# Kernel tuning notes

Hardware: AMD Instinct MI355X
Metric: run time of the kernel (lower is better)

Reference implementation:

```python
import jax, jax.numpy as jnp
import numpy as np
from jax import lax

# Static module config (matches init_kwargs)
KH, KW = 3, 3
SH, SW = 1, 1
PH, PW = 1, 1
DH, DW = 1, 1
DG = 1           # deformable groups
GROUPS = 1


def setup_inputs() -> dict:
    key = jax.random.key(0)
    k1, k2, k3 = jax.random.split(key, 3)
    B, C, H, W = 8, 256, 64, 64
    Co = 256
    K = KH * KW
    x = jax.random.normal(k1, (B, C, H, W), dtype=jnp.float32)
    # offset/mask conv weight: (2+1)*DG*K = 27 output channels; small so offsets are a few pixels
    w_offset = jax.random.normal(k2, (3 * DG * K, C, KH, KW), dtype=jnp.float32) * 0.05
    # main conv weight, uniform(-stdv, stdv) per reset_parameters
    stdv = 1.0 / np.sqrt(C * KH * KW)
    w_conv = jax.random.uniform(k3, (Co, C, KH, KW), dtype=jnp.float32, minval=-stdv, maxval=stdv)
    return {"input_feat": x, "w_offset": w_offset, "w_conv": w_conv}


def _bilinear_gather(x, py, px):
    """x: (B, DG, Cg, H, W); py/px: (B, DG, K, Ho, Wo) float sample coords.
    Returns sampled values (B, DG, Cg, K, Ho, Wo) with zero padding outside."""
    B, dg, Cg, H, W = x.shape
    _, _, K, Ho, Wo = py.shape
    xf = x.reshape(B, dg, Cg, H * W)

    y0 = jnp.floor(py)
    x0 = jnp.floor(px)
    ly = py - y0
    lx = px - x0
    y0i = y0.astype(jnp.int32)
    x0i = x0.astype(jnp.int32)
    y1i = y0i + 1
    x1i = x0i + 1

    def gather(yi, xi):
        valid = (yi >= 0) & (yi < H) & (xi >= 0) & (xi < W)
        idx = jnp.clip(yi, 0, H - 1) * W + jnp.clip(xi, 0, W - 1)  # (B,dg,K,Ho,Wo)
        idx_f = idx.reshape(B, dg, K * Ho * Wo)
        g = jax.vmap(jax.vmap(lambda f, i: jnp.take(f, i, axis=1)))(xf, idx_f)
        return g.reshape(B, dg, Cg, K, Ho, Wo), valid

    g00, v00 = gather(y0i, x0i)
    g01, v01 = gather(y0i, x1i)
    g10, v10 = gather(y1i, x0i)
    g11, v11 = gather(y1i, x1i)

    w00 = ((1 - ly) * (1 - lx) * v00)[:, :, None]
    w01 = ((1 - ly) * lx * v01)[:, :, None]
    w10 = (ly * (1 - lx) * v10)[:, :, None]
    w11 = (ly * lx * v11)[:, :, None]
    return g00 * w00 + g01 * w01 + g10 * w10 + g11 * w11


def _deform_conv(x, w_offset, w_conv):
    B, C, H, W = x.shape
    Co = w_conv.shape[0]
    K = KH * KW
    dn = ("NCHW", "OIHW", "NCHW")

    # offset/mask branch (regular conv)
    om = lax.conv_general_dilated(x, w_offset, (SH, SW), ((PH, PH), (PW, PW)),
                                  rhs_dilation=(DH, DW), dimension_numbers=dn)
    Ho, Wo = om.shape[2], om.shape[3]
    off_y = om[:, : DG * K].reshape(B, DG, K, Ho, Wo)
    off_x = om[:, DG * K: 2 * DG * K].reshape(B, DG, K, Ho, Wo)
    mask = jax.nn.sigmoid(om[:, 2 * DG * K:]).reshape(B, DG, 1, K, Ho, Wo)

    # base sampling grid
    oy = jnp.arange(Ho) * SH - PH                 # (Ho,)
    ox = jnp.arange(Wo) * SW - PW                 # (Wo,)
    ky = (jnp.arange(KH) * DH)[:, None].repeat(KW, 1).reshape(K)  # (K,)
    kx = (jnp.arange(KW) * DW)[None, :].repeat(KH, 0).reshape(K)  # (K,)
    py = ky[None, None, :, None, None] + oy[None, None, None, :, None] + off_y
    px = kx[None, None, :, None, None] + ox[None, None, None, None, :] + off_x

    xg = x.reshape(B, DG, C // DG, H, W)
    sampled = _bilinear_gather(xg, py, px) * mask  # (B,DG,Cg,K,Ho,Wo)

    cols = sampled.reshape(B, C, K, Ho * Wo)
    wk = w_conv.reshape(Co, C, K)
    out = jnp.einsum("bckn,ock->bon", cols, wk)
    return out.reshape(B, Co, Ho, Wo)


def reference(input_feat, w_offset, w_conv):
    return _deform_conv(input_feat, w_offset, w_conv)
```

## Files before the change

kernel.cpp:

```cpp
#include <hip/hip_runtime.h>
#include <hip/hip_bf16.h>

typedef float f32x4 __attribute__((ext_vector_type(4)));
typedef unsigned int u32x4 __attribute__((ext_vector_type(4)));
typedef __bf16 bf16x8 __attribute__((ext_vector_type(8)));

#define NSP 4096
#define KTOT 2304

static __device__ __forceinline__ float bflo(unsigned u) {
  return __builtin_bit_cast(float, u << 16);
}
static __device__ __forceinline__ float bfhi(unsigned u) {
  return __builtin_bit_cast(float, u & 0xffff0000u);
}
static __device__ __forceinline__ unsigned short bfbits(float f) {
  return __builtin_bit_cast(unsigned short, (__bf16)f);
}
static __device__ __forceinline__ unsigned packbf2(float f0, float f1) {
  return (unsigned)bfbits(f0) | ((unsigned)bfbits(f1) << 16);
}
static __device__ __forceinline__ float bf16f(unsigned short h) {
  return __builtin_bit_cast(float, (unsigned)h << 16);
}

__global__ __launch_bounds__(256) void k_nhwc(const float* __restrict__ x,
                                              unsigned short* __restrict__ XH) {
  const int by = blockIdx.x;
  const int t = threadIdx.x;
  const int xw = t & 63;
  const int cq = t >> 6;
  const float* xp = x + (((by >> 6) * 256 * 64 + (by & 63)) * 64 + xw);
  unsigned short* oh = XH + (by * 64 + xw) * 256;
#pragma unroll
  for (int j8 = 0; j8 < 8; ++j8) {
    const int c0 = cq * 64 + j8 * 8;
    u32x4 vh;
#pragma unroll
    for (int d = 0; d < 4; ++d) {
      float f0 = xp[(c0 + 2 * d) * 4096];
      float f1 = xp[(c0 + 2 * d + 1) * 4096];
      vh[d] = packbf2(f0, f1);
    }
    *(u32x4*)(oh + c0) = vh;
  }
}

__global__ void k_wprep_all(const float* __restrict__ wc, const float* __restrict__ wof,
                            unsigned short* __restrict__ AW2,
                            unsigned short* __restrict__ AF) {
  int idx = blockIdx.x * 256 + threadIdx.x;
  if (idx < 589824) {
    int ks = idx / 16384;
    int r = idx - ks * 16384;
    int chunk = r >> 5;
    int e = r & 31;
    int ah = chunk >> 8, am = chunk & 255;
    int col = (ks >> 2) * 256 + (ks & 3) * 64 + ah * 32 + e;
    int c = col & 255, tap = col >> 8;
    AW2[idx] = bfbits(wc[(am * 256 + c) * 9 + tap]);
  } else {
    int j = idx - 589824;
    if (j < 147456) {
      int skc = j >> 11;
      int r = j & 2047;
      int fi = r >> 9;
      int lane = (r >> 3) & 63;
      int e = r & 7;
      int ks = skc >> 1, kc = skc & 1;
      int tap = ks >> 2, q = ks & 3;
      int mr = lane & 15, ko = (lane >> 4) * 8;
      int m = (fi & 1) * 16 + mr;
      int gcol = tap * 256 + q * 64 + ko + kc * 32 + e;
      int c = gcol & 255;
      int t = gcol >> 8;
      float v = (m < 27) ? wof[(m * 256 + c) * 9 + t] : 0.f;
      unsigned short h = bfbits(v);
      AF[j] = (fi >> 1) ? bfbits(v - bf16f(h)) : h;
    }
  }
}

__global__ __launch_bounds__(256) void k_offc2(const unsigned short* __restrict__ AF,
                                               const unsigned short* __restrict__ XH,
                                               f32x4* __restrict__ W4,
                                               unsigned* __restrict__ C4) {
  __shared__ u32x4 ldsq[1024];
  unsigned char* ldsbase = (unsigned char*)ldsq;
  float* lds32 = (float*)ldsq;

  const int tid = threadIdx.x;
  const int bid = blockIdx.x;
  const int b = bid & 7;
  const int y = bid >> 3;
  const int l = tid & 63;
  const int w = tid >> 6;

  const unsigned short* xb = XH + b * (64 * 64 * 256);
  const int sp = tid >> 2;
  const int qtr = tid & 3;
  const unsigned swb = (unsigned)(sp & 7) << 4;
  const int col = w * 16 + (l & 15);
  const unsigned swc = (unsigned)(col & 7) << 4;

  f32x4 acc0 = (f32x4){0.f, 0.f, 0.f, 0.f};
  f32x4 acc1 = (f32x4){0.f, 0.f, 0.f, 0.f};
  u32x4 v0, v1;

  {
    const int yy = y - 1;
    const int xx = sp - 1;
    const bool valid = ((unsigned)yy < 64u) & ((unsigned)xx < 64u);
    const int yyc = min(max(yy, 0), 63), xxc = min(max(xx, 0), 63);
    const unsigned short* src = xb + ((yyc * 64 + xxc) * 256 + qtr * 16);
    u32x4 z = (u32x4){0u, 0u, 0u, 0u};
    v0 = valid ? *(const u32x4*)src : z;
    v1 = valid ? *(const u32x4*)(src + 8) : z;
    *(u32x4*)(ldsbase + (unsigned)sp * 128u + (((unsigned)(qtr * 32)) ^ swb)) = v0;
    *(u32x4*)(ldsbase + (unsigned)sp * 128u + (((unsigned)(qtr * 32 + 16)) ^ swb)) = v1;
  }

  for (int ks = 0; ks < 36; ++ks) {
    unsigned char* ldsB = ldsbase + (ks & 1) * 8192;
    unsigned char* ldsBn = ldsbase + ((ks & 1) ^ 1) * 8192;
    const bool pf = (ks + 1 < 36);

    if (pf) {
      int tap = (ks + 1) >> 2, q = (ks + 1) & 3;
      int yy = y + tap / 3 - 1, xx = sp + tap % 3 - 1;
      bool valid = ((unsigned)yy < 64u) & ((unsigned)xx < 64u);
      int yyc = min(max(yy, 0), 63), xxc = min(max(xx, 0), 63);
      const unsigned short* src = xb + ((yyc * 64 + xxc) * 256 + q * 64 + qtr * 16);
      u32x4 z = (u32x4){0u, 0u, 0u, 0u};
      v0 = valid ? *(const u32x4*)src : z;
      v1 = valid ? *(const u32x4*)(src + 8) : z;
    }

    asm volatile("s_waitcnt lgkmcnt(0)" ::: "memory");
    __builtin_amdgcn_s_barrier();

    const unsigned short* af = AF + ks * 4096;
#pragma unroll
    for (int kc = 0; kc < 2; ++kc) {
      bf16x8 ah0 = *(const bf16x8*)(af + kc * 2048 + l * 8);
      bf16x8 ah1 = *(const bf16x8*)(af + kc * 2048 + 512 + l * 8);
      bf16x8 al0 = *(const bf16x8*)(af + kc * 2048 + 1024 + l * 8);
      bf16x8 al1 = *(const bf16x8*)(af + kc * 2048 + 1536 + l * 8);
      bf16x8 bh = *(const bf16x8*)(ldsB + (unsigned)col * 128u +
                                   (((unsigned)(kc * 64 + (l >> 4) * 16)) ^ swc));
      acc0 = __builtin_amdgcn_mfma_f32_16x16x32_bf16(ah0, bh, acc0, 0, 0, 0);
      acc1 = __builtin_amdgcn_mfma_f32_16x16x32_bf16(ah1, bh, acc1, 0, 0, 0);
      acc0 = __builtin_amdgcn_mfma_f32_16x16x32_bf16(al0, bh, acc0, 0, 0, 0);
      acc1 = __builtin_amdgcn_mfma_f32_16x16x32_bf16(al1, bh, acc1, 0, 0, 0);
    }

    if (pf) {
      *(u32x4*)(ldsBn + (unsigned)sp * 128u + (((unsigned)(qtr * 32)) ^ swb)) = v0;
      *(u32x4*)(ldsBn + (unsigned)sp * 128u + (((unsigned)(qtr * 32 + 16)) ^ swb)) = v1;
    }
  }

  __syncthreads();
#pragma unroll
  for (int mf = 0; mf < 2; ++mf) {
    f32x4 a = mf ? acc1 : acc0;
#pragma unroll
    for (int r = 0; r < 4; ++r) {
      int m = mf * 16 + (l >> 4) * 4 + r;
      int px = w * 16 + (l & 15);
      lds32[m * 64 + px] = a[r];
    }
  }
  __syncthreads();

#pragma unroll
  for (int it = 0; it < 3; ++it) {
    int idx = tid + it * 256;
    if (idx < 9 * 64) {
      int k = idx >> 6, px = idx & 63;
      float oy = lds32[k * 64 + px];
      float ox = lds32[(9 + k) * 64 + px];
      float lg = lds32[(18 + k) * 64 + px];
      int s = y * 64 + px;
      float py = oy + (float)y - 1.f + (float)(k / 3);
      float pxf = ox + (float)px - 1.f + (float)(k % 3);
      float mk = 1.f / (1.f + __expf(-lg));

      float y0f = floorf(py), x0f = floorf(pxf);
      float ly = py - y0f, lx = pxf - x0f;
      int y0 = (int)y0f, x0 = (int)x0f;
      int y1 = y0 + 1, x1 = x0 + 1;
      float omy = 1.f - ly, omx = 1.f - lx;
      bool y0v = (unsigned)y0 < 64u, y1v = (unsigned)y1 < 64u;
      bool x0v = (unsigned)x0 < 64u, x1v = (unsigned)x1 < 64u;
      f32x4 wv;
      wv[0] = (y0v && x0v) ? omy * omx * mk : 0.f;
      wv[1] = (y0v && x1v) ? omy * lx * mk : 0.f;
      wv[2] = (y1v && x0v) ? ly * omx * mk : 0.f;
      wv[3] = (y1v && x1v) ? ly * lx * mk : 0.f;
      int y0c = min(max(y0, 0), 63), y1c = min(max(y1, 0), 63);
      int x0c = min(max(x0, 0), 63), x1c = min(max(x1, 0), 63);
      unsigned p00 = (unsigned)(y0c * 64 + x0c);
      unsigned p11 = (unsigned)(y1c * 64 + x1c);
      int ci = (b * 9 + k) * NSP + s;
      W4[ci] = wv;
      C4[ci] = p00 | (p11 << 16);
    }
  }
}

struct Bld16 {
  u32x4 g00a, g00b, g01a, g01b, g10a, g10b, g11a, g11b;
  f32x4 wv;
};

static __device__ __forceinline__ void loadB16(const unsigned short* __restrict__ xb,
                                               const f32x4* __restrict__ W4,
                                               const unsigned* __restrict__ C4,
                                               int b, int k, int c0, int bc, int s,
                                               Bld16& r) {
  int ci = (b * 9 + k) * NSP + s;
  r.wv = W4[ci];
  unsigned c4 = C4[ci];
  unsigned p00 = c4 & 0xffffu, p11 = c4 >> 16;
  unsigned p01 = (p00 & ~63u) | (p11 & 63u);
  unsigned p10 = (p11 & ~63u) | (p00 & 63u);
  const unsigned short* base = xb + (c0 + bc);
  const unsigned short* q00 = base + (p00 << 8);
  const unsigned short* q01 = base + (p01 << 8);
  const unsigned short* q10 = base + (p10 << 8);
  const unsigned short* q11 = base + (p11 << 8);
  r.g00a = *(const u32x4*)q00;
  r.g00b = *(const u32x4*)(q00 + 8);
  r.g01a = *(const u32x4*)q01;
  r.g01b = *(const u32x4*)(q01 + 8);
  r.g10a = *(const u32x4*)q10;
  r.g10b = *(const u32x4*)(q10 + 8);
  r.g11a = *(const u32x4*)q11;
  r.g11b = *(const u32x4*)(q11 + 8);
}

static __device__ __forceinline__ void blendB16(const Bld16& r, u32x4& o0, u32x4& o1) {
#pragma unroll
  for (int d = 0; d < 4; ++d) {
    float a0 = r.wv[0] * bflo(r.g00a[d]) + r.wv[1] * bflo(r.g01a[d]) +
               r.wv[2] * bflo(r.g10a[d]) + r.wv[3] * bflo(r.g11a[d]);
    float a1 = r.wv[0] * bfhi(r.g00a[d]) + r.wv[1] * bfhi(r.g01a[d]) +
               r.wv[2] * bfhi(r.g10a[d]) + r.wv[3] * bfhi(r.g11a[d]);
    o0[d] = packbf2(a0, a1);
    float b0 = r.wv[0] * bflo(r.g00b[d]) + r.wv[1] * bflo(r.g01b[d]) +
               r.wv[2] * bflo(r.g10b[d]) + r.wv[3] * bflo(r.g11b[d]);
    float b1 = r.wv[0] * bfhi(r.g00b[d]) + r.wv[1] * bfhi(r.g01b[d]) +
               r.wv[2] * bfhi(r.g10b[d]) + r.wv[3] * bfhi(r.g11b[d]);
    o1[d] = packbf2(b0, b1);
  }
}

__global__ __launch_bounds__(512) void k_gemm(const unsigned short* __restrict__ AW2,
                                              const unsigned short* __restrict__ XH,
                                              const f32x4* __restrict__ W4,
                                              const unsigned* __restrict__ C4,
                                              float* __restrict__ out) {
  __shared__ u32x4 lds2[2][3072];
  unsigned char* ldsbase = (unsigned char*)lds2;

  const int tid = threadIdx.x;
  const int bid = blockIdx.x;
  const int b = bid & 7;
  const int s0 = (bid >> 3) * 128;

  const int l = tid & 63;
  const int w = tid >> 6;
  const int wm = (w >> 1) * 64;
  const int wn = (w & 1) * 64;

  const int am = tid & 255;
  const int ah = tid >> 8;
  const unsigned swa = (unsigned)(am & 7) << 4;

  const int bn = tid >> 2;
  const int bc = (tid & 3) * 16;
  const int s = s0 + bn;
  const unsigned swb = (unsigned)(bn & 7) << 4;
  const unsigned short* xb = XH + b * (64 * 64 * 256);

  f32x4 acc[4][4];
#pragma unroll
  for (int i = 0; i < 4; ++i)
#pragma unroll
    for (int j = 0; j < 4; ++j) acc[i][j] = (f32x4){0.f, 0.f, 0.f, 0.f};

  u32x4 ar[4];
  u32x4 o0, o1;
  Bld16 bld;

#pragma unroll
  for (int j = 0; j < 4; ++j)
    ar[j] = *(const u32x4*)(AW2 + tid * 32 + j * 8);
  loadB16(xb, W4, C4, b, 0, 0, bc, s, bld);
  blendB16(bld, o0, o1);
  {
    unsigned char* ldsA = ldsbase;
    unsigned char* ldsB = ldsbase + 32768;
    const unsigned abase = (unsigned)am * 128u;
#pragma unroll
    for (int j = 0; j < 4; ++j)
      *(u32x4*)(ldsA + abase + (((unsigned)(ah * 64 + j * 16)) ^ swa)) = ar[j];
    const unsigned bbase = (unsigned)bn * 128u;
    *(u32x4*)(ldsB + bbase + (((unsigned)(bc * 2)) ^ swb)) = o0;
    *(u32x4*)(ldsB + bbase + (((unsigned)(bc * 2 + 16)) ^ swb)) = o1;
  }

  for (int ks = 0; ks < 36; ++ks) {
    const int cur = ks & 1;
    unsigned char* ldsA = ldsbase + cur * 49152;
    unsigned char* ldsB = ldsA + 32768;
    unsigned char* ldsAn = ldsbase + (cur ^ 1) * 49152;
    unsigned char* ldsBn = ldsAn + 32768;

    asm volatile("s_waitcnt lgkmcnt(0)" ::: "memory");
    __builtin_amdgcn_s_barrier();

    const int kn = (ks + 1) >> 2, cn = ((ks + 1) & 3) << 6;

    if (ks + 1 < 36) {
#pragma unroll
      for (int j = 0; j < 4; ++j)
        ar[j] = *(const u32x4*)(AW2 + (ks + 1) * 16384 + tid * 32 + j * 8);
    }

    __builtin_amdgcn_s_setprio(1);
    {
      bf16x8 af[4], bfr[4];
      const unsigned co = (unsigned)((l >> 4) * 16);
#pragma unroll
      for (int i = 0; i < 4; ++i) {
        int row = wm + i * 16 + (l & 15);
        af[i] = *(const bf16x8*)(ldsA + (unsigned)row * 128u +
                                 (co ^ ((unsigned)(row & 7) << 4)));
      }
#pragma unroll
      for (int j = 0; j < 4; ++j) {
        int col = wn + j * 16 + (l & 15);
        bfr[j] = *(const bf16x8*)(ldsB + (unsigned)col * 128u +
                                  (co ^ ((unsigned)(col & 7) << 4)));
      }
#pragma unroll
      for (int i = 0; i < 4; ++i)
#pragma unroll
        for (int j = 0; j < 4; ++j)
          acc[i][j] = __builtin_amdgcn_mfma_f32_16x16x32_bf16(af[i], bfr[j],
                                                              acc[i][j], 0, 0, 0);
    }
    __builtin_amdgcn_s_setprio(0);

    if (ks + 1 < 36) loadB16(xb, W4, C4, b, kn, cn, bc, s, bld);

    __builtin_amdgcn_s_setprio(1);
    {
      bf16x8 af[4], bfr[4];
      const unsigned co = (unsigned)(64 + (l >> 4) * 16);
#pragma unroll
      for (int i = 0; i < 4; ++i) {
        int row = wm + i * 16 + (l & 15);
        af[i] = *(const bf16x8*)(ldsA + (unsigned)row * 128u +
                                 (co ^ ((unsigned)(row & 7) << 4)));
      }
#pragma unroll
      for (int j = 0; j < 4; ++j) {
        int col = wn + j * 16 + (l & 15);
        bfr[j] = *(const bf16x8*)(ldsB + (unsigned)col * 128u +
                                  (co ^ ((unsigned)(col & 7) << 4)));
      }
#pragma unroll
      for (int i = 0; i < 4; ++i)
#pragma unroll
        for (int j = 0; j < 4; ++j)
          acc[i][j] = __builtin_amdgcn_mfma_f32_16x16x32_bf16(af[i], bfr[j],
                                                              acc[i][j], 0, 0, 0);
    }
    __builtin_amdgcn_s_setprio(0);

    if (ks + 1 < 36) {
      blendB16(bld, o0, o1);
      const unsigned abase = (unsigned)am * 128u;
#pragma unroll
      for (int j = 0; j < 4; ++j)
        *(u32x4*)(ldsAn + abase + (((unsigned)(ah * 64 + j * 16)) ^ swa)) = ar[j];
      const unsigned bbase = (unsigned)bn * 128u;
      *(u32x4*)(ldsBn + bbase + (((unsigned)(bc * 2)) ^ swb)) = o0;
      *(u32x4*)(ldsBn + bbase + (((unsigned)(bc * 2 + 16)) ^ swb)) = o1;
    }
  }

  const int cn2 = l & 15;
  const int r0 = (l >> 4) * 4;
#pragma unroll
  for (int i = 0; i < 4; ++i) {
#pragma unroll
    for (int j = 0; j < 4; ++j) {
      int sc = s0 + wn + j * 16 + cn2;
#pragma unroll
      for (int r = 0; r < 4; ++r) {
        int o = wm + i * 16 + r0 + r;
        out[((b * 256 + o) << 12) + sc] = acc[i][j][r];
      }
    }
  }
}

extern "C" void kernel_launch(void* const* d_in, const int* in_sizes, int n_in,
                              void* d_out, int out_size, void* d_ws, size_t ws_size,
                              hipStream_t stream) {
  const float* x = (const float*)d_in[0];
  const float* wof = (const float*)d_in[1];
  const float* wc = (const float*)d_in[2];
  float* out = (float*)d_out;
  char* ws = (char*)d_ws;

  unsigned short* XH = (unsigned short*)(ws);
  unsigned short* AW2 = (unsigned short*)(ws + 16777216);
  unsigned short* AF = (unsigned short*)(ws + 17956864);
  f32x4* W4 = (f32x4*)(ws + 18251776);
  unsigned* C4 = (unsigned*)(ws + 22970368);

  k_nhwc<<<512, 256, 0, stream>>>(x, XH);
  k_wprep_all<<<2880, 256, 0, stream>>>(wc, wof, AW2, AF);
  k_offc2<<<512, 256, 0, stream>>>(AF, XH, W4, C4);
  k_gemm<<<256, 512, 0, stream>>>(AW2, XH, W4, C4, out);
}
```

Baseline: 126.5 us.

## Deepen global prefetch pipeline to two stages with decoupled metadata loads

Splits the B-operand load into a metadata load (weights and corner indices) and a corner gather. The main loop is unrolled by two with ping-pong register sets so that the gather for step ks+2 and the metadata for ks+3 are issued while step ks computes. This is meant to hide the dependent latency chain from metadata load to corner gather, and the global load latency in general, behind the MFMA work. The cost is roughly double the register state for prefetch buffers, which may raise VGPR pressure or cause spills at 512 threads per block.

```diff
diff --git a/kernel.cpp b/kernel.cpp
--- a/kernel.cpp
+++ b/kernel.cpp
@@ -214,14 +214,19 @@
   f32x4 wv;
 };
 
-static __device__ __forceinline__ void loadB16(const unsigned short* __restrict__ xb,
-                                               const f32x4* __restrict__ W4,
-                                               const unsigned* __restrict__ C4,
-                                               int b, int k, int c0, int bc, int s,
-                                               Bld16& r) {
+static __device__ __forceinline__ void loadMeta(const f32x4* __restrict__ W4,
+                                                const unsigned* __restrict__ C4,
+                                                int b, int k, int s,
+                                                f32x4& wv, unsigned& c4) {
   int ci = (b * 9 + k) * NSP + s;
-  r.wv = W4[ci];
-  unsigned c4 = C4[ci];
+  wv = W4[ci];
+  c4 = C4[ci];
+}
+
+static __device__ __forceinline__ void loadCorners(const unsigned short* __restrict__ xb,
+                                                   f32x4 wv, unsigned c4, int c0, int bc,
+                                                   Bld16& r) {
+  r.wv = wv;
   unsigned p00 = c4 & 0xffffu, p11 = c4 >> 16;
   unsigned p01 = (p00 & ~63u) | (p11 & 63u);
   unsigned p10 = (p11 & ~63u) | (p00 & 63u);
@@ -259,7 +264,7 @@
 __global__ __launch_bounds__(512) void k_gemm(const unsigned short* __restrict__ AW2,
                                               const unsigned short* __restrict__ XH,
                                               const f32x4* __restrict__ W4,
-                                              const unsigned* __restrict__ C4,
+                                              const unsigned* __restrict__ C4v,
                                               float* __restrict__ out) {
   __shared__ u32x4 lds2[2][3072];
   unsigned char* ldsbase = (unsigned char*)lds2;
@@ -290,107 +295,104 @@
 #pragma unroll
     for (int j = 0; j < 4; ++j) acc[i][j] = (f32x4){0.f, 0.f, 0.f, 0.f};
 
-  u32x4 ar[4];
-  u32x4 o0, o1;
-  Bld16 bld;
-
-#pragma unroll
-  for (int j = 0; j < 4; ++j)
-    ar[j] = *(const u32x4*)(AW2 + tid * 32 + j * 8);
-  loadB16(xb, W4, C4, b, 0, 0, bc, s, bld);
-  blendB16(bld, o0, o1);
+  f32x4 mwvA, mwvB;
+  unsigned mc4A, mc4B;
+  Bld16 bldA, bldB;
+  u32x4 arA[4], arB[4];
+
+  loadMeta(W4, C4v, b, 0, s, mwvA, mc4A);
+  loadMeta(W4, C4v, b, 0, s, mwvB, mc4B);
+#pragma unroll
+  for (int j = 0; j < 4; ++j) arA[j] = *(const u32x4*)(AW2 + tid * 32 + j * 8);
+  loadCorners(xb, mwvA, mc4A, 0, bc, bldA);
+  loadMeta(W4, C4v, b, 0, s, mwvA, mc4A);
   {
+    u32x4 o0, o1;
+    blendB16(bldA, o0, o1);
     unsigned char* ldsA = ldsbase;
     unsigned char* ldsB = ldsbase + 32768;
     const unsigned abase = (unsigned)am * 128u;
 #pragma unroll
     for (int j = 0; j < 4; ++j)
-      *(u32x4*)(ldsA + abase + (((unsigned)(ah * 64 + j * 16)) ^ swa)) = ar[j];
+      *(u32x4*)(ldsA + abase + (((unsigned)(ah * 64 + j * 16)) ^ swa)) = arA[j];
     const unsigned bbase = (unsigned)bn * 128u;
     *(u32x4*)(ldsB + bbase + (((unsigned)(bc * 2)) ^ swb)) = o0;
     *(u32x4*)(ldsB + bbase + (((unsigned)(bc * 2 + 16)) ^ swb)) = o1;
   }
-
-  for (int ks = 0; ks < 36; ++ks) {
-    const int cur = ks & 1;
+#pragma unroll
+  for (int j = 0; j < 4; ++j)
+    arB[j] = *(const u32x4*)(AW2 + 16384 + tid * 32 + j * 8);
+  loadCorners(xb, mwvB, mc4B, 64, bc, bldB);
+
+  auto mfma_half = [&](unsigned char* ldsA, unsigned char* ldsB, int H) {
+    bf16x8 af[4], bfr[4];
+    const unsigned co = (unsigned)(H * 64 + ((l >> 4) * 16));
+#pragma unroll
+    for (int i = 0; i < 4; ++i) {
+      int row = wm + i * 16 + (l & 15);
+      af[i] = *(const bf16x8*)(ldsA + (unsigned)row * 128u +
+                               (co ^ ((unsigned)(row & 7) << 4)));
+    }
+#pragma unroll
+    for (int j = 0; j < 4; ++j) {
+      int col = wn + j * 16 + (l & 15);
+      bfr[j] = *(const bf16x8*)(ldsB + (unsigned)col * 128u +
+                                (co ^ ((unsigned)(col & 7) << 4)));
+    }
+#pragma unroll
+    for (int i = 0; i < 4; ++i)
+#pragma unroll
+      for (int j = 0; j < 4; ++j)
+        acc[i][j] = __builtin_amdgcn_mfma_f32_16x16x32_bf16(af[i], bfr[j],
+                                                            acc[i][j], 0, 0, 0);
+  };
+
+  auto gstep = [&](int KS, u32x4 (&arI)[4], Bld16& bldI, f32x4& mwvI, unsigned& mc4I,
+                   f32x4& mwvO, unsigned& mc4O, u32x4 (&arU)[4], Bld16& bldU) {
+    const int cur = KS & 1;
     unsigned char* ldsA = ldsbase + cur * 49152;
     unsigned char* ldsB = ldsA + 32768;
     unsigned char* ldsAn = ldsbase + (cur ^ 1) * 49152;
     unsigned char* ldsBn = ldsAn + 32768;
 
+    if (KS + 2 < 36) {
+#pragma unroll
+      for (int j = 0; j < 4; ++j)
+        arI[j] = *(const u32x4*)(AW2 + (KS + 2) * 16384 + tid * 32 + j * 8);
+    }
+
     asm volatile("s_waitcnt lgkmcnt(0)" ::: "memory");
     __builtin_amdgcn_s_barrier();
 
-    const int kn = (ks + 1) >> 2, cn = ((ks + 1) & 3) << 6;
-
-    if (ks + 1 < 36) {
+    __builtin_amdgcn_s_setprio(1);
+    mfma_half(ldsA, ldsB, 0);
+    __builtin_amdgcn_s_setprio(0);
+
+    if (KS + 2 < 36)
+      loadCorners(xb, mwvI, mc4I, ((KS + 2) & 3) << 6, bc, bldI);
+    if (KS + 3 < 36)
+      loadMeta(W4, C4v, b, (KS + 3) >> 2, s, mwvO, mc4O);
+
+    __builtin_amdgcn_s_setprio(1);
+    mfma_half(ldsA, ldsB, 1);
+    __builtin_amdgcn_s_setprio(0);
+
+    if (KS + 1 < 36) {
+      u32x4 o0, o1;
+      blendB16(bldU, o0, o1);
+      const unsigned abase = (unsigned)am * 128u;
 #pragma unroll
       for (int j = 0; j < 4; ++j)
-        ar[j] = *(const u32x4*)(AW2 + (ks + 1) * 16384 + tid * 32 + j * 8);
-    }
-
-    __builtin_amdgcn_s_setprio(1);
-    {
-      bf16x8 af[4], bfr[4];
-      const unsigned co = (unsigned)((l >> 4) * 16);
-#pragma unroll
-      for (int i = 0; i < 4; ++i) {
-        int row = wm + i * 16 + (l & 15);
-        af[i] = *(const bf16x8*)(ldsA + (unsigned)row * 128u +
-                                 (co ^ ((unsigned)(row & 7) << 4)));
-      }
-#pragma unroll
-      for (int j = 0; j < 4; ++j) {
-        int col = wn + j * 16 + (l & 15);
-        bfr[j] = *(const bf16x8*)(ldsB + (unsigned)col * 128u +
-                                  (co ^ ((unsigned)(col & 7) << 4)));
-      }
-#pragma unroll
-      for (int i = 0; i < 4; ++i)
-#pragma unroll
-        for (int j = 0; j < 4; ++j)
-          acc[i][j] = __builtin_amdgcn_mfma_f32_16x16x32_bf16(af[i], bfr[j],
-                                                              acc[i][j], 0, 0, 0);
-    }
-    __builtin_amdgcn_s_setprio(0);
-
-    if (ks + 1 < 36) loadB16(xb, W4, C4, b, kn, cn, bc, s, bld);
-
-    __builtin_amdgcn_s_setprio(1);
-    {
-      bf16x8 af[4], bfr[4];
-      const unsigned co = (unsigned)(64 + (l >> 4) * 16);
-#pragma unroll
-      for (int i = 0; i < 4; ++i) {
-        int row = wm + i * 16 + (l & 15);
-        af[i] = *(const bf16x8*)(ldsA + (unsigned)row * 128u +
-                                 (co ^ ((unsigned)(row & 7) << 4)));
-      }
-#pragma unroll
-      for (int j = 0; j < 4; ++j) {
-        int col = wn + j * 16 + (l & 15);
-        bfr[j] = *(const bf16x8*)(ldsB + (unsigned)col * 128u +
-                                  (co ^ ((unsigned)(col & 7) << 4)));
-      }
-#pragma unroll
-      for (int i = 0; i < 4; ++i)
-#pragma unroll
-        for (int j = 0; j < 4; ++j)
-          acc[i][j] = __builtin_amdgcn_mfma_f32_16x16x32_bf16(af[i], bfr[j],
-                                                              acc[i][j], 0, 0, 0);
-    }
-    __builtin_amdgcn_s_setprio(0);
-
-    if (ks + 1 < 36) {
-      blendB16(bld, o0, o1);
-      const unsigned abase = (unsigned)am * 128u;
-#pragma unroll
-      for (int j = 0; j < 4; ++j)
-        *(u32x4*)(ldsAn + abase + (((unsigned)(ah * 64 + j * 16)) ^ swa)) = ar[j];
+        *(u32x4*)(ldsAn + abase + (((unsigned)(ah * 64 + j * 16)) ^ swa)) = arU[j];
       const unsigned bbase = (unsigned)bn * 128u;
       *(u32x4*)(ldsBn + bbase + (((unsigned)(bc * 2)) ^ swb)) = o0;
       *(u32x4*)(ldsBn + bbase + (((unsigned)(bc * 2 + 16)) ^ swb)) = o1;
     }
+  };
+
+  for (int ks2 = 0; ks2 < 36; ks2 += 2) {
+    gstep(ks2, arA, bldA, mwvA, mc4A, mwvB, mc4B, arB, bldB);
+    gstep(ks2 + 1, arB, bldB, mwvB, mc4B, mwvA, mc4A, arA, bldA);
   }
 
   const int cn2 = l & 15;
```

New measurement: 121.6 us. 1.04x faster.
